# Kernel optimization log

Hardware: AMD Instinct MI355X
Metric: run time of the kernel (lower is better)

## Reference

```python
import jax, jax.numpy as jnp
import numpy as np

B, N = 32, 50000
E = 200000
D, D_LG = 64, 256
M_ALL, M_MEM = 100000, 80000
NUM_VI_SEG = 80000


def _dense(key, din, dout):
    k1, k2 = jax.random.split(key)
    lim = 1.0 / np.sqrt(din)
    W = jax.random.uniform(k1, (din, dout), jnp.float32, -lim, lim)
    b = jax.random.uniform(k2, (dout,), jnp.float32, -lim, lim)
    return W, b


def setup_inputs() -> dict:
    key = jax.random.key(0)
    ks = jax.random.split(key, 16)
    rng = np.random.RandomState(0)

    eg = np.sort(rng.randint(0, B, E)).astype(np.int32)
    vi = rng.randint(0, N, E).astype(np.int32)
    vj = rng.randint(0, N, E).astype(np.int32)
    rel = rng.randint(0, 200, E).astype(np.int32)
    seg_vi = np.sort(rng.randint(0, NUM_VI_SEG, E)).astype(np.int32)
    seg_vj = rng.randint(0, E, E).astype(np.int32)
    e2vi = rng.randint(0, M_ALL, E).astype(np.int32)
    e2vj = rng.randint(0, M_ALL, E).astype(np.int32)
    scanned_edges = jnp.asarray(np.stack([eg, vi, vj, rel, seg_vi, seg_vj, e2vi, e2vj], axis=1))

    new_idx = np.sort(rng.choice(M_ALL, M_MEM, replace=False)).astype(np.int32)[:, None]

    W_h, b_h = _dense(ks[0], D, D)
    W_hlg, b_hlg = _dense(ks[1], D_LG, D)
    W_rlg, b_rlg = _dense(ks[2], D_LG, D)
    Wl0, bl0 = _dense(ks[3], D, D)
    Wr0, br0 = _dense(ks[4], D, D)
    Wl1, bl1 = _dense(ks[5], 2 * D, D)
    Wr1, br1 = _dense(ks[6], 2 * D, D)

    return {
        'node_attention': jax.random.uniform(ks[7], (B, N), jnp.float32),
        'edges_y': jax.random.uniform(ks[8], (E,), jnp.float32),
        'hidden_uncon': jax.random.normal(ks[9], (1, N, D_LG), jnp.float32),
        'hidden_con': jax.random.normal(ks[10], (M_MEM, D), jnp.float32),
        'query_head_emb': jax.random.normal(ks[11], (B, D_LG), jnp.float32),
        'query_rel_emb': jax.random.normal(ks[12], (B, D_LG), jnp.float32),
        'W_h': W_h, 'b_h': b_h, 'W_hlg': W_hlg, 'b_hlg': b_hlg,
        'W_rlg': W_rlg, 'b_rlg': b_rlg,
        'Wl0': Wl0, 'bl0': bl0, 'Wr0': Wr0, 'br0': br0,
        'Wl1': Wl1, 'bl1': bl1, 'Wr1': Wr1, 'br1': br1,
        'scanned_edges': scanned_edges,
        'new_idx_for_memorized': jnp.asarray(new_idx),
        'n_memorized_and_scanned_nodes': M_ALL,
    }


def _segment_softmax(logits, seg, num_seg):
    # numerically-stable sparse softmax over sorted vi-segments
    m = jax.ops.segment_max(logits, seg, num_segments=num_seg)
    e = jnp.exp(logits - m[seg])
    s = jax.ops.segment_sum(e, seg, num_segments=num_seg)
    return e / s[seg]


def reference(node_attention, edges_y, hidden_uncon, hidden_con,
              query_head_emb, query_rel_emb,
              W_h, b_h, W_hlg, b_hlg, W_rlg, b_rlg,
              Wl0, bl0, Wr0, br0, Wl1, bl1, Wr1, br1,
              scanned_edges, new_idx_for_memorized, n_memorized_and_scanned_nodes):
    Bv, Nv = node_attention.shape
    eg = scanned_edges[:, 0]
    vi = scanned_edges[:, 1]
    vj = scanned_edges[:, 2]
    seg_vi = scanned_edges[:, 4]
    e2vi = scanned_edges[:, 6]
    e2vj = scanned_edges[:, 7]

    # proj_for_hidden, scatter memorized states to memorized+scanned slots
    hc = jnp.tanh(hidden_con @ W_h + b_h)                        # M_mem x D
    hc_full = jnp.zeros((n_memorized_and_scanned_nodes, hc.shape[-1]), hc.dtype)
    hc_full = hc_full.at[new_idx_for_memorized[:, 0]].set(hc)    # M_all x D

    hu = jnp.tanh(hidden_uncon @ W_hlg + b_hlg)
    qh = jnp.tanh(query_head_emb @ W_hlg + b_hlg)                # B x D (use_ent_emb)
    qr = jnp.tanh(query_rel_emb @ W_rlg + b_rlg)                 # B x D
    qv = qh + qr

    # node2edge gathers (context = conditioned + unconditioned hidden)
    h_vi = hc_full[e2vi] + hu[0, vi]                             # E x D
    h_vj = hc_full[e2vj] + hu[0, vj]                             # E x D
    q_e = qv[eg]                                                 # E x D

    # transition_fn G with interact [[[0],[1]], [[0,2],[1,2]]]
    l0 = jnp.tanh(h_vi @ Wl0 + bl0)
    r0 = jnp.tanh(h_vj @ Wr0 + br0)
    l1 = jnp.tanh(jnp.concatenate([h_vi, q_e], -1) @ Wl1 + bl1)
    r1 = jnp.tanh(jnp.concatenate([h_vj, q_e], -1) @ Wr1 + br1)
    logits = jnp.sum(l0 * r0, -1) + jnp.sum(l1 * r1, -1)         # E

    # neighbor softmax at vi, modulated by edges_y
    trans = _segment_softmax(logits, seg_vi, NUM_VI_SEG) * edges_y

    # flow: gather attention at vi, aggregate(sum) scatter to (eg_idx, vj)
    flow = node_attention[eg, vi] * trans
    new_att = jnp.zeros((Bv, Nv), flow.dtype).at[eg, vj].add(flow)
    return new_att
```

## Files before the change

kernel.cpp:

```cpp
#include <hip/hip_runtime.h>


typedef __attribute__((ext_vector_type(8))) short s16x8;
typedef __attribute__((ext_vector_type(4))) float f32x4;
typedef __attribute__((ext_vector_type(8))) unsigned short u16x8;

__device__ __forceinline__ float fast_tanh(float x) {
    float e = __expf(2.0f * x);
    return 1.0f - 2.0f * __builtin_amdgcn_rcpf(e + 1.0f);
}

__device__ __forceinline__ unsigned short bf16r(float f) {
    unsigned int u = __float_as_uint(f);
    u = (u + 0x7fffu + ((u >> 16) & 1u)) >> 16;
    return (unsigned short)u;
}
__device__ __forceinline__ float bf16f(unsigned short h) {
    return __uint_as_float(((unsigned int)h) << 16);
}
__device__ __forceinline__ float blo(unsigned int u) {
    return __uint_as_float(u << 16);
}
__device__ __forceinline__ float bhi(unsigned int u) {
    return __uint_as_float(u & 0xffff0000u);
}

__device__ __forceinline__ int saddr(int row, int chunk) {
    return (row << 6) + ((chunk ^ (row & 7)) << 2);
}

__global__ void k_scatter_inv(const int* __restrict__ new_idx, int* __restrict__ inv, int M) {
    int i = blockIdx.x * blockDim.x + threadIdx.x;
    if (i < M) inv[new_idx[i]] = i;
}

__global__ void k_pack(const float* __restrict__ Wl0, const float* __restrict__ Wl1,
                       const float* __restrict__ Wr0, const float* __restrict__ Wr1,
                       unsigned short* __restrict__ Bp) {
    int tid = blockIdx.x * blockDim.x + threadIdx.x;
    if (tid >= 2048) return;
    int lane = tid & 63;
    int ks = (tid >> 6) & 1;
    int g = tid >> 7;
    int col = g * 16 + (lane & 15);
    int kb = ks * 32 + (lane >> 4) * 8;
    const float* W = (col < 64) ? Wl0 : (col < 128) ? Wl1 : (col < 192) ? Wr0 : Wr1;
    int c = col & 63;
    #pragma unroll
    for (int i = 0; i < 8; ++i) {
        float w = W[(kb + i) * 64 + c];
        unsigned short hi = bf16r(w);
        unsigned short lo = bf16r(w - bf16f(hi));
        Bp[(size_t)tid * 8 + i] = hi;
        Bp[16384 + (size_t)tid * 8 + i] = lo;
    }
}

__global__ void k_q(const float* __restrict__ qhe, const float* __restrict__ qre,
                    const float* __restrict__ W_hlg, const float* __restrict__ b_hlg,
                    const float* __restrict__ W_rlg, const float* __restrict__ b_rlg,
                    const float* __restrict__ Wl1, const float* __restrict__ bl1,
                    const float* __restrict__ Wr1, const float* __restrict__ br1,
                    float* __restrict__ ql1b, float* __restrict__ qr1b) {
    __shared__ float qv_s[64];
    int b = blockIdx.x, d = threadIdx.x;
    float ah = 0.f, ar = 0.f;
    for (int k = 0; k < 256; ++k) {
        ah += qhe[b * 256 + k] * W_hlg[k * 64 + d];
        ar += qre[b * 256 + k] * W_rlg[k * 64 + d];
    }
    qv_s[d] = fast_tanh(ah + b_hlg[d]) + fast_tanh(ar + b_rlg[d]);
    __syncthreads();
    float a1 = 0.f, a2 = 0.f;
    for (int k = 0; k < 64; ++k) {
        float v = qv_s[k];
        a1 += v * Wl1[(64 + k) * 64 + d];
        a2 += v * Wr1[(64 + k) * 64 + d];
    }
    ql1b[b * 64 + d] = a1 + bl1[d];
    qr1b[b * 64 + d] = a2 + br1[d];
}

__device__ __forceinline__ void s1_batch(const float* __restrict__ s, int lane, int b4,
                                         const float* __restrict__ Wbase, int wu,
                                         float acc1[16]) {
    f32x4 xrow[4];
    #pragma unroll
    for (int j = 0; j < 4; ++j)
        xrow[j] = *reinterpret_cast<const f32x4*>(&s[saddr(lane, b4 * 4 + j)]);
    #pragma unroll
    for (int k4 = 0; k4 < 4; ++k4) {
        #pragma unroll
        for (int kk = 0; kk < 4; ++kk) {
            float xk = xrow[k4][kk];
            const float* wrow = Wbase + ((b4 * 4 + k4) * 4 + kk) * 64 + wu * 16;
            #pragma unroll
            for (int c = 0; c < 16; ++c) acc1[c] = __builtin_fmaf(xk, wrow[c], acc1[c]);
        }
    }
}

__global__ __launch_bounds__(256, 6) void k_tab(
        const float* __restrict__ Xc, const float* __restrict__ Xu,
        const float* __restrict__ W_h, const float* __restrict__ b_h,
        const float* __restrict__ W_hlg, const float* __restrict__ b_hlg,
        const float* __restrict__ bl0, const float* __restrict__ br0,
        const unsigned short* __restrict__ Bp,
        unsigned short* __restrict__ Ahc, unsigned short* __restrict__ Ahu,
        int M, int N, int HUB) {
    __shared__ float s[64 * 64];
    __shared__ unsigned short dstage[16 * 264];
    unsigned short* hhi = reinterpret_cast<unsigned short*>(s);

    const int t = threadIdx.x;
    const int wu = __builtin_amdgcn_readfirstlane(t >> 6);
    const int lane = t & 63;

    const int bid = (int)blockIdx.x;
    const int TB = (int)gridDim.x;
    const long hb = ((long)bid * HUB) / TB;
    const bool hc = (((long)(bid + 1) * HUB) / TB) == hb;
    const int idx = hc ? (bid - (int)hb) : (int)hb;

    float acc1[16];
    #pragma unroll
    for (int c = 0; c < 16; ++c) acc1[c] = 0.f;

    int base, rows;
    const float* bias;
    unsigned short* table;

    if (hc) {
        base = idx * 64;
        rows = (M - base < 64) ? (M - base) : 64;
        bias = b_h;
        table = Ahc;
        #pragma unroll
        for (int i = 0; i < 4; ++i) {
            int f = i * 256 + t;
            int r = f >> 4, ch = f & 15;
            float4 v = make_float4(0.f, 0.f, 0.f, 0.f);
            if (r < rows) v = *reinterpret_cast<const float4*>(Xc + (size_t)(base + r) * 64 + (ch << 2));
            *reinterpret_cast<float4*>(&s[saddr(r, ch)]) = v;
        }
        __syncthreads();
        __builtin_amdgcn_s_setprio(1);
        for (int b4 = 0; b4 < 4; ++b4)
            s1_batch(s, lane, b4, W_h, wu, acc1);
        __builtin_amdgcn_s_setprio(0);
    } else {
        base = idx * 64;
        rows = (N - base < 64) ? (N - base) : 64;
        bias = b_hlg;
        table = Ahu;
        float4 xr[4];
        #pragma unroll
        for (int i = 0; i < 4; ++i) {
            int f = i * 256 + t;
            int r = f >> 4, ch = f & 15;
            xr[i] = make_float4(0.f, 0.f, 0.f, 0.f);
            if (r < rows)
                xr[i] = *reinterpret_cast<const float4*>(Xu + (size_t)(base + r) * 256 + (ch << 2));
        }
        for (int kc = 0; kc < 4; ++kc) {
            __syncthreads();
            #pragma unroll
            for (int i = 0; i < 4; ++i) {
                int f = i * 256 + t;
                int r = f >> 4, ch = f & 15;
                *reinterpret_cast<float4*>(&s[saddr(r, ch)]) = xr[i];
            }
            __syncthreads();
            if (kc + 1 < 4) {
                #pragma unroll
                for (int i = 0; i < 4; ++i) {
                    int f = i * 256 + t;
                    int r = f >> 4, ch = f & 15;
                    if (r < rows)
                        xr[i] = *reinterpret_cast<const float4*>(
                            Xu + (size_t)(base + r) * 256 + (kc + 1) * 64 + (ch << 2));
                }
            }
            const float* Wb = W_hlg + (size_t)kc * 64 * 64;
            __builtin_amdgcn_s_setprio(1);
            for (int b4 = 0; b4 < 4; ++b4)
                s1_batch(s, lane, b4, Wb, wu, acc1);
            __builtin_amdgcn_s_setprio(0);
        }
    }

    __syncthreads();
    {
        unsigned short hi[16];
        #pragma unroll
        for (int c = 0; c < 16; ++c)
            hi[c] = bf16r(fast_tanh(acc1[c] + bias[wu * 16 + c]));
        int o = lane * 68 + wu * 16;
        #pragma unroll
        for (int c = 0; c < 16; ++c) hhi[o + c] = hi[c];
    }
    __syncthreads();

    const s16x8* Bph = reinterpret_cast<const s16x8*>(Bp);
    const s16x8* Bpl = reinterpret_cast<const s16x8*>(Bp + 16384);
    const int l15 = lane & 15, l4 = lane >> 4;
    for (int rt = 0; rt < 4; ++rt) {
        int arow = (rt * 16 + l15) * 68 + l4 * 8;
        s16x8 a0v = *reinterpret_cast<const s16x8*>(&hhi[arow]);
        s16x8 a1v = *reinterpret_cast<const s16x8*>(&hhi[arow + 32]);
        #pragma unroll
        for (int ct = 0; ct < 4; ++ct) {
            int g = wu * 4 + ct;
            s16x8 bh0 = Bph[(g * 2 + 0) * 64 + lane];
            s16x8 bh1 = Bph[(g * 2 + 1) * 64 + lane];
            s16x8 bl0v = Bpl[(g * 2 + 0) * 64 + lane];
            s16x8 bl1v = Bpl[(g * 2 + 1) * 64 + lane];
            f32x4 acc = {0.f, 0.f, 0.f, 0.f};
            acc = __builtin_amdgcn_mfma_f32_16x16x32_bf16(a0v, bh0, acc, 0, 0, 0);
            acc = __builtin_amdgcn_mfma_f32_16x16x32_bf16(a1v, bh1, acc, 0, 0, 0);
            acc = __builtin_amdgcn_mfma_f32_16x16x32_bf16(a0v, bl0v, acc, 0, 0, 0);
            acc = __builtin_amdgcn_mfma_f32_16x16x32_bf16(a1v, bl1v, acc, 0, 0, 0);
            float badd = 0.f;
            if (!hc) {
                if (g < 4) badd = bl0[g * 16 + l15];
                else if (g >= 8 && g < 12) badd = br0[(g - 8) * 16 + l15];
            }
            int side = g >> 3, which = (g >> 2) & 1;
            int x = (g & 3) * 16 + l15;
            int pos = side * 128 + x * 2 + which;
            #pragma unroll
            for (int r = 0; r < 4; ++r)
                dstage[(l4 * 4 + r) * 264 + pos] = bf16r(acc[r] + badd);
        }
        __syncthreads();
        #pragma unroll
        for (int it = 0; it < 2; ++it) {
            int f = (it * 256 + t) * 8;
            int row = f >> 8, off = f & 255;
            u16x8 v = *reinterpret_cast<const u16x8*>(&dstage[row * 264 + off]);
            int grow = rt * 16 + row;
            if (grow < rows)
                *reinterpret_cast<u16x8*>(&table[(size_t)(base + grow) * 256 + off]) = v;
        }
        __syncthreads();
    }
}

__global__ void k_edge(const int* __restrict__ se, const int* __restrict__ inv,
                       const unsigned int* __restrict__ Ahc, const unsigned int* __restrict__ Ahu,
                       const float* __restrict__ ql1b, const float* __restrict__ qr1b,
                       const float* __restrict__ ey, const float* __restrict__ natt,
                       float* __restrict__ trans, float* __restrict__ psum,
                       int2* __restrict__ aux, int E, int N, int ZROW) {
    int tid = blockIdx.x * blockDim.x + threadIdx.x;
    int e = tid >> 4;
    int sl = tid & 15;
    if (e >= E) return;
    const int4* sr = reinterpret_cast<const int4*>(se + (size_t)e * 8);
    int4 ra = sr[0], rb = sr[1];
    int eg = ra.x, vi = ra.y, vj = ra.z, seg = rb.x, e2vi = rb.z, e2vj = rb.w;
    int ii = inv[e2vi]; ii = (ii < 0) ? ZROW : ii;
    int ij = inv[e2vj]; ij = (ij < 0) ? ZROW : ij;
    uint4 a  = *reinterpret_cast<const uint4*>(Ahc + (size_t)ii * 128 + sl * 4);
    uint4 b  = *reinterpret_cast<const uint4*>(Ahu + (size_t)vi * 128 + sl * 4);
    uint4 c  = *reinterpret_cast<const uint4*>(Ahc + (size_t)ij * 128 + 64 + sl * 4);
    uint4 d4 = *reinterpret_cast<const uint4*>(Ahu + (size_t)vj * 128 + 64 + sl * 4);
    float4 q1 = *reinterpret_cast<const float4*>(ql1b + eg * 64 + sl * 4);
    float4 q2 = *reinterpret_cast<const float4*>(qr1b + eg * 64 + sl * 4);
    float acc = 0.f;
    #pragma unroll
    for (int j = 0; j < 4; ++j) {
        unsigned int av = (&a.x)[j], bv = (&b.x)[j];
        unsigned int cv = (&c.x)[j], dv = (&d4.x)[j];
        float l0 = fast_tanh(blo(av) + blo(bv));
        float l1 = fast_tanh(bhi(av) + bhi(bv) + (&q1.x)[j]);
        float r0 = fast_tanh(blo(cv) + blo(dv));
        float r1 = fast_tanh(bhi(cv) + bhi(dv) + (&q2.x)[j]);
        acc = __builtin_fmaf(l0, r0, acc);
        acc = __builtin_fmaf(l1, r1, acc);
    }
    #pragma unroll
    for (int off = 8; off; off >>= 1) acc += __shfl_xor(acc, off);
    if (sl == 0) {
        float ex = __expf(acc);
        trans[e] = ex * ey[e] * natt[(size_t)eg * N + vi];
        aux[e] = make_int2(eg * N + vj, seg);
        atomicAdd(&psum[seg], ex);
    }
}

__global__ void k_final(const int2* __restrict__ aux, const float* __restrict__ trans,
                        const float* __restrict__ psum, float* __restrict__ out, int E) {
    int e = blockIdx.x * blockDim.x + threadIdx.x;
    if (e >= E) return;
    int2 a = aux[e];
    float t = trans[e] * __builtin_amdgcn_rcpf(psum[a.y]);
    atomicAdd(&out[a.x], t);
}

extern "C" void kernel_launch(void* const* d_in, const int* in_sizes, int n_in,
                              void* d_out, int out_size, void* d_ws, size_t ws_size,
                              hipStream_t stream) {
    const float* natt  = (const float*)d_in[0];
    const float* ey    = (const float*)d_in[1];
    const float* h_unc = (const float*)d_in[2];
    const float* h_con = (const float*)d_in[3];
    const float* qhe   = (const float*)d_in[4];
    const float* qre   = (const float*)d_in[5];
    const float* W_h   = (const float*)d_in[6];
    const float* b_h   = (const float*)d_in[7];
    const float* W_hlg = (const float*)d_in[8];
    const float* b_hlg = (const float*)d_in[9];
    const float* W_rlg = (const float*)d_in[10];
    const float* b_rlg = (const float*)d_in[11];
    const float* Wl0   = (const float*)d_in[12];
    const float* bl0   = (const float*)d_in[13];
    const float* Wr0   = (const float*)d_in[14];
    const float* br0   = (const float*)d_in[15];
    const float* Wl1   = (const float*)d_in[16];
    const float* bl1   = (const float*)d_in[17];
    const float* Wr1   = (const float*)d_in[18];
    const float* br1   = (const float*)d_in[19];
    const int* se      = (const int*)d_in[20];
    const int* new_idx = (const int*)d_in[21];

    const int B     = 32;
    const int N     = in_sizes[0] / B;
    const int E     = in_sizes[20] / 8;
    const int M_MEM = in_sizes[21];
    const int M_ALL = 100000;
    const int NSEG  = 80000;

    char* ws = (char*)d_ws;
    size_t off = 0;
    unsigned short* Ahc = (unsigned short*)(ws + off);  off += (size_t)(M_MEM + 1) * 256 * 2;
    unsigned short* Ahu = (unsigned short*)(ws + off);  off += (size_t)N * 256 * 2;
    int* inv = (int*)(ws + off);            off += (size_t)M_ALL * 4;
    float* trans = (float*)(ws + off);      off += (size_t)E * 4;
    float* psum = (float*)(ws + off);       off += (size_t)NSEG * 4;
    int2* aux = (int2*)(ws + off);          off += (size_t)E * 8;
    float* ql1b = (float*)(ws + off);       off += (size_t)B * 64 * 4;
    float* qr1b = (float*)(ws + off);       off += (size_t)B * 64 * 4;
    unsigned short* Bpack = (unsigned short*)(ws + off); off += (size_t)2 * 16384 * 2;

    hipMemsetAsync(d_out, 0, (size_t)out_size * 4, stream);
    hipMemsetAsync(inv, 0xFF, (size_t)M_ALL * 4, stream);
    hipMemsetAsync(psum, 0, (size_t)NSEG * 4, stream);
    hipMemsetAsync(Ahc + (size_t)M_MEM * 256, 0, 256 * 2, stream);

    const int HCB = (M_MEM + 63) / 64;
    const int HUB = (N + 63) / 64;

    k_scatter_inv<<<(M_MEM + 255) / 256, 256, 0, stream>>>(new_idx, inv, M_MEM);
    k_pack<<<8, 256, 0, stream>>>(Wl0, Wl1, Wr0, Wr1, Bpack);
    k_q<<<B, 64, 0, stream>>>(qhe, qre, W_hlg, b_hlg, W_rlg, b_rlg,
                              Wl1, bl1, Wr1, br1, ql1b, qr1b);
    k_tab<<<HCB + HUB, 256, 0, stream>>>(h_con, h_unc, W_h, b_h, W_hlg, b_hlg,
                                         bl0, br0, Bpack, Ahc, Ahu, M_MEM, N, HUB);
    k_edge<<<((size_t)E * 16 + 255) / 256, 256, 0, stream>>>(se, inv, (const unsigned int*)Ahc,
                                                (const unsigned int*)Ahu, ql1b, qr1b,
                                                ey, natt, trans, psum, aux, E, N, M_MEM);
    k_final<<<(E + 255) / 256, 256, 0, stream>>>(aux, trans, psum, (float*)d_out, E);
}
```

Measured before the change: 139.2 us.

## Load input rows directly from global memory instead of staging through LDS

The first-stage GEMV in k_tab now has each lane read its own input row straight from global memory with f32x4 loads. Previously the block did a coalesced cooperative load into swizzled shared memory, with barriers between stages. This removes the LDS staging, the swizzle, several __syncthreads and the 16KB float scratch, which may raise occupancy. The trade-off is uncoalesced per-lane strided global loads, where the four waves of a block each re-read the same rows, and no software prefetch of the next K chunk.

```diff
diff --git a/kernel.cpp b/kernel.cpp
--- a/kernel.cpp
+++ b/kernel.cpp
@@ -23,10 +23,6 @@
 }
 __device__ __forceinline__ float bhi(unsigned int u) {
     return __uint_as_float(u & 0xffff0000u);
-}
-
-__device__ __forceinline__ int saddr(int row, int chunk) {
-    return (row << 6) + ((chunk ^ (row & 7)) << 2);
 }
 
 __global__ void k_scatter_inv(const int* __restrict__ new_idx, int* __restrict__ inv, int M) {
@@ -81,19 +77,22 @@
     qr1b[b * 64 + d] = a2 + br1[d];
 }
 
-__device__ __forceinline__ void s1_batch(const float* __restrict__ s, int lane, int b4,
-                                         const float* __restrict__ Wbase, int wu,
-                                         float acc1[16]) {
+__device__ __forceinline__ void s1_batch_g(const float* __restrict__ xg, bool rok,
+                                           int koff,
+                                           const float* __restrict__ Wbase, int wu,
+                                           float acc1[16]) {
     f32x4 xrow[4];
     #pragma unroll
-    for (int j = 0; j < 4; ++j)
-        xrow[j] = *reinterpret_cast<const f32x4*>(&s[saddr(lane, b4 * 4 + j)]);
+    for (int j = 0; j < 4; ++j) {
+        xrow[j] = (f32x4){0.f, 0.f, 0.f, 0.f};
+        if (rok) xrow[j] = *reinterpret_cast<const f32x4*>(xg + koff + j * 4);
+    }
     #pragma unroll
     for (int k4 = 0; k4 < 4; ++k4) {
         #pragma unroll
         for (int kk = 0; kk < 4; ++kk) {
             float xk = xrow[k4][kk];
-            const float* wrow = Wbase + ((b4 * 4 + k4) * 4 + kk) * 64 + wu * 16;
+            const float* wrow = Wbase + (koff + k4 * 4 + kk) * 64 + wu * 16;
             #pragma unroll
             for (int c = 0; c < 16; ++c) acc1[c] = __builtin_fmaf(xk, wrow[c], acc1[c]);
         }
@@ -108,9 +107,8 @@
         const unsigned short* __restrict__ Bp,
         unsigned short* __restrict__ Ahc, unsigned short* __restrict__ Ahu,
         int M, int N, int HUB) {
-    __shared__ float s[64 * 64];
+    __shared__ unsigned short hhi[64 * 68];
     __shared__ unsigned short dstage[16 * 264];
-    unsigned short* hhi = reinterpret_cast<unsigned short*>(s);
 
     const int t = threadIdx.x;
     const int wu = __builtin_amdgcn_readfirstlane(t >> 6);
@@ -135,61 +133,31 @@
         rows = (M - base < 64) ? (M - base) : 64;
         bias = b_h;
         table = Ahc;
-        #pragma unroll
-        for (int i = 0; i < 4; ++i) {
-            int f = i * 256 + t;
-            int r = f >> 4, ch = f & 15;
-            float4 v = make_float4(0.f, 0.f, 0.f, 0.f);
-            if (r < rows) v = *reinterpret_cast<const float4*>(Xc + (size_t)(base + r) * 64 + (ch << 2));
-            *reinterpret_cast<float4*>(&s[saddr(r, ch)]) = v;
-        }
-        __syncthreads();
+        const float* xg = Xc + (size_t)(base + lane) * 64;
+        const bool rok = lane < rows;
         __builtin_amdgcn_s_setprio(1);
+        #pragma unroll 1
         for (int b4 = 0; b4 < 4; ++b4)
-            s1_batch(s, lane, b4, W_h, wu, acc1);
+            s1_batch_g(xg, rok, b4 * 16, W_h, wu, acc1);
         __builtin_amdgcn_s_setprio(0);
     } else {
         base = idx * 64;
         rows = (N - base < 64) ? (N - base) : 64;
         bias = b_hlg;
         table = Ahu;
-        float4 xr[4];
-        #pragma unroll
-        for (int i = 0; i < 4; ++i) {
-            int f = i * 256 + t;
-            int r = f >> 4, ch = f & 15;
-            xr[i] = make_float4(0.f, 0.f, 0.f, 0.f);
-            if (r < rows)
-                xr[i] = *reinterpret_cast<const float4*>(Xu + (size_t)(base + r) * 256 + (ch << 2));
+        const float* xg = Xu + (size_t)(base + lane) * 256;
+        const bool rok = lane < rows;
+        __builtin_amdgcn_s_setprio(1);
+        #pragma unroll 1
+        for (int kc = 0; kc < 4; ++kc) {
+            const float* Wb = W_hlg + (size_t)kc * 64 * 64;
+            #pragma unroll 1
+            for (int b4 = 0; b4 < 4; ++b4)
+                s1_batch_g(xg + kc * 64, rok, b4 * 16, Wb, wu, acc1);
         }
-        for (int kc = 0; kc < 4; ++kc) {
-            __syncthreads();
-            #pragma unroll
-            for (int i = 0; i < 4; ++i) {
-                int f = i * 256 + t;
-                int r = f >> 4, ch = f & 15;
-                *reinterpret_cast<float4*>(&s[saddr(r, ch)]) = xr[i];
-            }
-            __syncthreads();
-            if (kc + 1 < 4) {
-                #pragma unroll
-                for (int i = 0; i < 4; ++i) {
-                    int f = i * 256 + t;
-                    int r = f >> 4, ch = f & 15;
-                    if (r < rows)
-                        xr[i] = *reinterpret_cast<const float4*>(
-                            Xu + (size_t)(base + r) * 256 + (kc + 1) * 64 + (ch << 2));
-                }
-            }
-            const float* Wb = W_hlg + (size_t)kc * 64 * 64;
-            __builtin_amdgcn_s_setprio(1);
-            for (int b4 = 0; b4 < 4; ++b4)
-                s1_batch(s, lane, b4, Wb, wu, acc1);
-            __builtin_amdgcn_s_setprio(0);
-        }
-    }
-
-    __syncthreads();
+        __builtin_amdgcn_s_setprio(0);
+    }
+
     {
         unsigned short hi[16];
         #pragma unroll
```

After: 162.8 us. 17.0% more time.
